# Kernel optimization log

Measured on AMD Instinct MI355X. Metric: run time of the kernel, lower is better.

Reference implementation:

```python
import jax, jax.numpy as jnp
import numpy as np
import math

B, S, DIN, DOUT, H, L, R, E = 8, 512, 256, 256, 8, 4, 8, 65536
N = B * S  # graph nodes = all tokens
DEPTH = DOUT // H


def setup_inputs() -> dict:
    key = jax.random.key(0)
    ks = jax.random.split(key, 16)
    s_in = 1.0 / math.sqrt(DIN)
    s_out = 1.0 / math.sqrt(DOUT)
    return {
        "x": jax.random.normal(ks[0], (B, S, DIN), jnp.float32),
        # graph structure (constant ints)
        "edge_src": jax.random.randint(ks[1], (E,), 0, N),
        "edge_dst": jax.random.randint(ks[2], (E,), 0, N),
        "edge_type": jax.random.randint(ks[3], (E,), 0, R),
        # linear: input_size -> output_size
        "Wl": jax.random.normal(ks[4], (DOUT, DIN), jnp.float32) * s_in,
        "bl": jnp.zeros((DOUT,), jnp.float32),
        # relational GAT params per layer / relation
        "Wgat": jax.random.normal(ks[5], (L, R, DOUT, DOUT), jnp.float32) * s_out,
        "a_src": jax.random.normal(ks[6], (L, R, DOUT), jnp.float32) * s_out,
        "a_dst": jax.random.normal(ks[7], (L, R, DOUT), jnp.float32) * s_out,
        # linear1: output_size -> input_size
        "W1": jax.random.normal(ks[8], (DIN, DOUT), jnp.float32) * s_out,
        "b1": jnp.zeros((DIN,), jnp.float32),
        # Wq, Wk: input_size -> output_size
        "Wq": jax.random.normal(ks[9], (DOUT, DIN), jnp.float32) * s_in,
        "bq": jnp.zeros((DOUT,), jnp.float32),
        "Wk": jax.random.normal(ks[10], (DOUT, DIN), jnp.float32) * s_in,
        "bk": jnp.zeros((DOUT,), jnp.float32),
    }


def _segment_softmax(e, dst, n):
    m = jax.ops.segment_max(e, dst, num_segments=n)
    ex = jnp.exp(e - m[dst])
    denom = jax.ops.segment_sum(ex, dst, num_segments=n)
    return ex / (denom[dst] + 1e-16)


def _rgat(h, Wgat, a_src, a_dst, edge_src, edge_dst, edge_type):
    # h: [N, DOUT]
    for l in range(L):
        # per-relation transform of all nodes: [R, N, D]
        hr = jnp.einsum('nd,rde->rne', h, Wgat[l])
        msg = hr[edge_type, edge_src]  # [E, D] gather by (relation, src)
        logits = (jnp.sum(a_src[l][edge_type] * msg, axis=-1)
                  + jnp.sum(a_dst[l][edge_type] * h[edge_dst], axis=-1))
        alpha = _segment_softmax(jax.nn.leaky_relu(logits, 0.2), edge_dst, N)
        agg = jax.ops.segment_sum(alpha[:, None] * msg, edge_dst, num_segments=N)
        h = jax.nn.elu(agg)
    return h


def reference(x, edge_src, edge_dst, edge_type, Wl, bl, Wgat, a_src, a_dst,
              W1, b1, Wq, bq, Wk, bk):
    h = x @ Wl.T + bl                       # [B, S, DOUT]
    h = h.reshape(N, DOUT)
    h = _rgat(h, Wgat, a_src, a_dst, edge_src, edge_dst, edge_type)
    h = h.reshape(B, S, DOUT)
    h = h @ W1.T + b1                       # [B, S, DIN]
    q = (h @ Wq.T + bq).reshape(B, S, H, DEPTH).transpose(0, 2, 1, 3)
    k = (h @ Wk.T + bk).reshape(B, S, H, DEPTH).transpose(0, 2, 1, 3)
    attn = jnp.einsum('bhqd,bhkd->bhqk', q, k) / math.sqrt(DEPTH)
    return attn
```

## Files before the change

kernel.cpp:

```cpp
#include <hip/hip_runtime.h>
#include <math.h>

#define NN 4096
#define D 256
#define RR 8
#define LL 4
#define EE 65536
#define BB 8
#define SS 512
#define HH 8

typedef short bf16x8 __attribute__((ext_vector_type(8)));
typedef float f32x4 __attribute__((ext_vector_type(4)));

__device__ __forceinline__ unsigned short f2bf(float f) {
  unsigned u = __float_as_uint(f);
  unsigned r = (u + 0x7fffu + ((u >> 16) & 1u)) >> 16;
  return (unsigned short)r;
}
__device__ __forceinline__ float bf2f(unsigned short s) {
  return __uint_as_float(((unsigned)s) << 16);
}

__device__ __forceinline__ void gload16(unsigned short* dst, const unsigned short* src) {
  __builtin_amdgcn_global_load_lds(
      (const __attribute__((address_space(1))) void*)src,
      (__attribute__((address_space(3))) void*)dst, 16, 0, 0);
}

template<int BM, int BN, bool F32OUT, bool SPLITOUT>
__global__ __launch_bounds__(256) void gemm_split(
    const unsigned short* __restrict__ Ah, const unsigned short* __restrict__ Al,
    const unsigned short* __restrict__ Bh, const unsigned short* __restrict__ Bl,
    const float* __restrict__ bias,
    float* __restrict__ C, unsigned short* __restrict__ Ch, unsigned short* __restrict__ Cl,
    int M, int N, int K)
{
  constexpr int MF = BM / 32;
  constexpr int NF = BN / 32;
  __shared__ unsigned short lds[2 * (BM + BN) * 32];
  unsigned short* lA = lds;
  unsigned short* lB = lds + 2 * BM * 32;

  const int t = threadIdx.x;
  const int lane = t & 63;
  const int w = t >> 6;
  const int wm = w >> 1, wn = w & 1;
  const int rb = blockIdx.y * BM;
  const int cb = blockIdx.x * BN;

  f32x4 acc[MF][NF];
#pragma unroll
  for (int m = 0; m < MF; ++m)
#pragma unroll
    for (int n = 0; n < NF; ++n)
      acc[m][n] = (f32x4){0.f, 0.f, 0.f, 0.f};

  const int srow = t >> 2, sslot = t & 3;
  const unsigned short* gAh = Ah + (size_t)(rb + srow) * K + sslot * 8;
  const unsigned short* gAl = Al + (size_t)(rb + srow) * K + sslot * 8;
  const unsigned short* gBh = Bh + (size_t)(cb + srow) * K + sslot * 8;
  const unsigned short* gBl = Bl + (size_t)(cb + srow) * K + sslot * 8;

  for (int k0 = 0; k0 < K; k0 += 32) {
#pragma unroll
    for (int i = 0; i < BM / 64; ++i) {
      gload16(lA + i * 2048 + t * 8,           gAh + (size_t)i * 64 * K + k0);
      gload16(lA + BM * 32 + i * 2048 + t * 8, gAl + (size_t)i * 64 * K + k0);
    }
#pragma unroll
    for (int i = 0; i < BN / 64; ++i) {
      gload16(lB + i * 2048 + t * 8,           gBh + (size_t)i * 64 * K + k0);
      gload16(lB + BN * 32 + i * 2048 + t * 8, gBl + (size_t)i * 64 * K + k0);
    }
    __syncthreads();

    bf16x8 ah[MF], al[MF];
#pragma unroll
    for (int m = 0; m < MF; ++m) {
      int off = (wm * (BM / 2) + m * 16 + (lane & 15)) * 32 + (lane >> 4) * 8;
      ah[m] = *(const bf16x8*)(lA + off);
      al[m] = *(const bf16x8*)(lA + BM * 32 + off);
    }
#pragma unroll
    for (int n = 0; n < NF; ++n) {
      int boff = (wn * (BN / 2) + n * 16 + (lane & 15)) * 32 + (lane >> 4) * 8;
      bf16x8 bh = *(const bf16x8*)(lB + boff);
      bf16x8 bl = *(const bf16x8*)(lB + BN * 32 + boff);
#pragma unroll
      for (int m = 0; m < MF; ++m) {
        acc[m][n] = __builtin_amdgcn_mfma_f32_16x16x32_bf16(ah[m], bh, acc[m][n], 0, 0, 0);
        acc[m][n] = __builtin_amdgcn_mfma_f32_16x16x32_bf16(al[m], bh, acc[m][n], 0, 0, 0);
        acc[m][n] = __builtin_amdgcn_mfma_f32_16x16x32_bf16(ah[m], bl, acc[m][n], 0, 0, 0);
      }
    }
    __syncthreads();
  }

#pragma unroll
  for (int m = 0; m < MF; ++m) {
#pragma unroll
    for (int n = 0; n < NF; ++n) {
      int row0 = rb + wm * (BM / 2) + m * 16 + (lane >> 4) * 4;
      int col = cb + wn * (BN / 2) + n * 16 + (lane & 15);
      float bv = bias ? bias[col] : 0.f;
#pragma unroll
      for (int j = 0; j < 4; ++j) {
        float v = acc[m][n][j] + bv;
        size_t idx = (size_t)(row0 + j) * N + col;
        if (F32OUT) C[idx] = v;
        if (SPLITOUT) {
          unsigned short hb = f2bf(v);
          Ch[idx] = hb;
          Cl[idx] = f2bf(v - bf2f(hb));
        }
      }
    }
  }
}

__global__ __launch_bounds__(256) void cvt_split_k(const float* __restrict__ src,
    unsigned short* __restrict__ hi, unsigned short* __restrict__ lo, int n4)
{
  int i = blockIdx.x * 256 + threadIdx.x;
  if (i >= n4) return;
  float4 v = ((const float4*)src)[i];
  ushort4 h, l;
  h.x = f2bf(v.x); l.x = f2bf(v.x - bf2f(h.x));
  h.y = f2bf(v.y); l.y = f2bf(v.y - bf2f(h.y));
  h.z = f2bf(v.z); l.z = f2bf(v.z - bf2f(h.z));
  h.w = f2bf(v.w); l.w = f2bf(v.w - bf2f(h.w));
  ((ushort4*)hi)[i] = h;
  ((ushort4*)lo)[i] = l;
}

__global__ __launch_bounds__(256) void transp_split_k(const float* __restrict__ W,
    unsigned short* __restrict__ th, unsigned short* __restrict__ tl)
{
  __shared__ float s[32][33];
  int g = blockIdx.z, bi = blockIdx.y, bj = blockIdx.x;
  int t = threadIdx.x;
  int r = t >> 3, c = (t & 7) * 4;
  float4 v = *(const float4*)(W + ((size_t)g * D + bi * 32 + r) * D + bj * 32 + c);
  s[r][c + 0] = v.x; s[r][c + 1] = v.y; s[r][c + 2] = v.z; s[r][c + 3] = v.w;
  __syncthreads();
  size_t ob = ((size_t)g * D + bj * 32 + r) * D + bi * 32 + c;
  ushort4 h, l;
  float o0 = s[c + 0][r], o1 = s[c + 1][r], o2 = s[c + 2][r], o3 = s[c + 3][r];
  h.x = f2bf(o0); l.x = f2bf(o0 - bf2f(h.x));
  h.y = f2bf(o1); l.y = f2bf(o1 - bf2f(h.y));
  h.z = f2bf(o2); l.z = f2bf(o2 - bf2f(h.z));
  h.w = f2bf(o3); l.w = f2bf(o3 - bf2f(h.w));
  *(ushort4*)(th + ob) = h;
  *(ushort4*)(tl + ob) = l;
}

__global__ void count_k(const int* __restrict__ ed, int* __restrict__ cnt) {
  int e = blockIdx.x * 256 + threadIdx.x;
  if (e < EE) atomicAdd(&cnt[ed[e]], 1);
}

__global__ __launch_bounds__(1024) void scan_k(const int* __restrict__ cnt,
    int* __restrict__ off, int* __restrict__ cur) {
  __shared__ int part[1024];
  int t = threadIdx.x;
  int base = t * 4;
  int c0 = cnt[base], c1 = cnt[base+1], c2 = cnt[base+2], c3 = cnt[base+3];
  int s = c0 + c1 + c2 + c3;
  part[t] = s;
  __syncthreads();
  for (int o = 1; o < 1024; o <<= 1) {
    int v = 0;
    if (t >= o) v = part[t - o];
    __syncthreads();
    part[t] += v;
    __syncthreads();
  }
  int excl = part[t] - s;
  off[base] = excl; off[base+1] = excl + c0; off[base+2] = excl + c0 + c1;
  off[base+3] = excl + c0 + c1 + c2;
  cur[base] = excl; cur[base+1] = excl + c0; cur[base+2] = excl + c0 + c1;
  cur[base+3] = excl + c0 + c1 + c2;
  if (t == 1023) off[NN] = EE;
}

__global__ void fill_k(const int* __restrict__ ed, int* __restrict__ cur,
                       int* __restrict__ csr) {
  int e = blockIdx.x * 256 + threadIdx.x;
  if (e < EE) { int p = atomicAdd(&cur[ed[e]], 1); csr[p] = e; }
}

__global__ __launch_bounds__(256) void wa_all_k(const float* __restrict__ Wg,
    const float* __restrict__ asrc, float* __restrict__ wa)
{
  int wid = blockIdx.x * 4 + (threadIdx.x >> 6);
  int lane = threadIdx.x & 63;
  int lr = wid >> 8, d = wid & 255;
  const float* row = Wg + ((size_t)lr * D + d) * D;
  const float* av = asrc + (size_t)lr * D;
  float s = 0.f;
  for (int i = lane; i < D; i += 64) s += row[i] * av[i];
#pragma unroll
  for (int o = 32; o; o >>= 1) s += __shfl_down(s, o);
  if (lane == 0) wa[wid] = s;
}

__global__ __launch_bounds__(256) void fold_k(const float* __restrict__ Wq,
    const float* __restrict__ Wk, const float* __restrict__ W1,
    unsigned short* __restrict__ fh, unsigned short* __restrict__ fl)
{
  int j = (blockIdx.x & 3) * 64 + (threadIdx.x & 63);
  int i = (blockIdx.x >> 2) * 4 + (threadIdx.x >> 6);
  const float* row = i < 256 ? Wq + (size_t)i * D : Wk + (size_t)(i - 256) * D;
  float s = 0.f;
  for (int k = 0; k < D; ++k) s += row[k] * W1[(size_t)k * D + j];
  size_t idx = (size_t)i * D + j;
  unsigned short hb = f2bf(s);
  fh[idx] = hb;
  fl[idx] = f2bf(s - bf2f(hb));
}

__global__ __launch_bounds__(256) void foldb_k(const float* __restrict__ Wq,
    const float* __restrict__ Wk, const float* __restrict__ b1,
    const float* __restrict__ bq, const float* __restrict__ bk,
    float* __restrict__ bqk)
{
  int idx = blockIdx.x * 4 + (threadIdx.x >> 6);
  int lane = threadIdx.x & 63;
  const float* row = idx < 256 ? Wq + (size_t)idx * D : Wk + (size_t)(idx - 256) * D;
  float s = 0.f;
  for (int i = lane; i < D; i += 64) s += row[i] * b1[i];
#pragma unroll
  for (int o = 32; o; o >>= 1) s += __shfl_down(s, o);
  if (lane == 0) bqk[idx] = s + (idx < 256 ? bq[idx] : bk[idx - 256]);
}

__global__ __launch_bounds__(256) void scores2_k(const float* __restrict__ h,
    const float* __restrict__ wa, const float* __restrict__ adst,
    float* __restrict__ ssrc, float* __restrict__ sdst)
{
  int n = blockIdx.x;
  int w = threadIdx.x >> 6, lane = threadIdx.x & 63;
  float4 hv = ((const float4*)(h + (size_t)n * D))[lane];
#pragma unroll
  for (int rr = 0; rr < 2; ++rr) {
    int r = w * 2 + rr;
    float4 a = ((const float4*)(wa + (size_t)r * D))[lane];
    float4 b = ((const float4*)(adst + (size_t)r * D))[lane];
    float s1 = hv.x*a.x + hv.y*a.y + hv.z*a.z + hv.w*a.w;
    float s2 = hv.x*b.x + hv.y*b.y + hv.z*b.z + hv.w*b.w;
#pragma unroll
    for (int o = 32; o; o >>= 1) { s1 += __shfl_down(s1, o); s2 += __shfl_down(s2, o); }
    if (lane == 0) { ssrc[(size_t)r * NN + n] = s1; sdst[(size_t)r * NN + n] = s2; }
  }
}

__global__ __launch_bounds__(256) void agg_fused_k(
    const int* __restrict__ csr, const int* __restrict__ off,
    const int* __restrict__ et, const int* __restrict__ es,
    const float* __restrict__ ssrc, const float* __restrict__ sdst,
    const float* __restrict__ hr2,
    unsigned short* __restrict__ hh, unsigned short* __restrict__ hl,
    const float* __restrict__ wa_next, const float* __restrict__ adst_next,
    float* __restrict__ ssrc_o, float* __restrict__ sdst_o)
{
  __shared__ float slog[1024];
  __shared__ int soff[1024];
  __shared__ float sdn[RR];
  __shared__ float red[8];
  int n = blockIdx.x, tid = threadIdx.x;
  int o0 = off[n];
  int deg = off[n + 1] - o0;
  if (deg > 1024) deg = 1024;
  if (tid < RR) sdn[tid] = sdst[(size_t)tid * NN + n];
  __syncthreads();
  for (int i = tid; i < deg; i += 256) {
    int e = csr[o0 + i];
    int t = et[e], s = es[e];
    float v = ssrc[(size_t)t * NN + s] + sdn[t];
    slog[i] = v > 0.f ? v : 0.2f * v;
    soff[i] = s * (RR * D) + t * D;
  }
  __syncthreads();
  int lane = tid & 63, wv = tid >> 6;
  float lm = -INFINITY;
  for (int i = tid; i < deg; i += 256) lm = fmaxf(lm, slog[i]);
#pragma unroll
  for (int o = 32; o; o >>= 1) lm = fmaxf(lm, __shfl_xor(lm, o));
  if (lane == 0) red[wv] = lm;
  __syncthreads();
  float m = fmaxf(fmaxf(red[0], red[1]), fmaxf(red[2], red[3]));
  float ls = 0.f;
  for (int i = tid; i < deg; i += 256) {
    float a = expf(slog[i] - m);
    slog[i] = a;
    ls += a;
  }
#pragma unroll
  for (int o = 32; o; o >>= 1) ls += __shfl_xor(ls, o);
  if (lane == 0) red[4 + wv] = ls;
  __syncthreads();
  float dinv = 1.f / (red[4] + red[5] + red[6] + red[7] + 1e-16f);
  float acc = 0.f;
  for (int i = 0; i < deg; ++i)
    acc += slog[i] * hr2[(size_t)soff[i] + tid];
  acc *= dinv;
  float v = acc > 0.f ? acc : expm1f(acc);
  size_t idx = (size_t)n * D + tid;
  unsigned short hb = f2bf(v);
  hh[idx] = hb;
  hl[idx] = f2bf(v - bf2f(hb));

  if (wa_next) {
    __syncthreads();
    slog[tid] = v;
    __syncthreads();
#pragma unroll
    for (int rr2 = 0; rr2 < 2; ++rr2) {
      int r = wv * 2 + rr2;
      const float* wr = wa_next + (size_t)r * D;
      const float* ar = adst_next + (size_t)r * D;
      float s1 = slog[lane] * wr[lane] + slog[lane+64] * wr[lane+64]
               + slog[lane+128] * wr[lane+128] + slog[lane+192] * wr[lane+192];
      float s2 = slog[lane] * ar[lane] + slog[lane+64] * ar[lane+64]
               + slog[lane+128] * ar[lane+128] + slog[lane+192] * ar[lane+192];
#pragma unroll
      for (int o = 32; o; o >>= 1) { s1 += __shfl_down(s1, o); s2 += __shfl_down(s2, o); }
      if (lane == 0) { ssrc_o[(size_t)r * NN + n] = s1; sdst_o[(size_t)r * NN + n] = s2; }
    }
  }
}

__global__ __launch_bounds__(256) void attn_mfma_k(
    const unsigned short* __restrict__ qkh, const unsigned short* __restrict__ qkl,
    float* __restrict__ out)
{
  int bh = blockIdx.y; int b = bh >> 3, hd = bh & 7;
  int rb = (blockIdx.x >> 3) * 64, cb = (blockIdx.x & 7) * 64;
  int t = threadIdx.x, lane = t & 63, w = t >> 6;
  int wm = w >> 1, wn = w & 1;
  int colq = hd * 32 + (lane >> 4) * 8;
  int colk = 256 + colq;
  int arow = b * SS + rb + wm * 32 + (lane & 15);
  int brow = b * SS + cb + wn * 32 + (lane & 15);

  bf16x8 aH[2], aL[2], bH[2], bL[2];
#pragma unroll
  for (int m = 0; m < 2; ++m) {
    size_t o1 = (size_t)(arow + m * 16) * 512 + colq;
    aH[m] = *(const bf16x8*)(qkh + o1);
    aL[m] = *(const bf16x8*)(qkl + o1);
    size_t o2 = (size_t)(brow + m * 16) * 512 + colk;
    bH[m] = *(const bf16x8*)(qkh + o2);
    bL[m] = *(const bf16x8*)(qkl + o2);
  }
  f32x4 acc[2][2];
#pragma unroll
  for (int m = 0; m < 2; ++m)
#pragma unroll
    for (int n = 0; n < 2; ++n) {
      acc[m][n] = (f32x4){0.f, 0.f, 0.f, 0.f};
      acc[m][n] = __builtin_amdgcn_mfma_f32_16x16x32_bf16(aH[m], bH[n], acc[m][n], 0, 0, 0);
      acc[m][n] = __builtin_amdgcn_mfma_f32_16x16x32_bf16(aL[m], bH[n], acc[m][n], 0, 0, 0);
      acc[m][n] = __builtin_amdgcn_mfma_f32_16x16x32_bf16(aH[m], bL[n], acc[m][n], 0, 0, 0);
    }
  const float scale = 0.17677669529663687f;
  size_t ob = (size_t)bh * SS * SS;
#pragma unroll
  for (int m = 0; m < 2; ++m)
#pragma unroll
    for (int n = 0; n < 2; ++n) {
      int row0 = rb + wm * 32 + m * 16 + (lane >> 4) * 4;
      int col = cb + wn * 32 + n * 16 + (lane & 15);
#pragma unroll
      for (int j = 0; j < 4; ++j)
        out[ob + (size_t)(row0 + j) * SS + col] = acc[m][n][j] * scale;
    }
}

extern "C" void kernel_launch(void* const* d_in, const int* in_sizes, int n_in,
                              void* d_out, int out_size, void* d_ws, size_t ws_size,
                              hipStream_t stream) {
  const float* x    = (const float*)d_in[0];
  const int*   es   = (const int*)d_in[1];
  const int*   ed   = (const int*)d_in[2];
  const int*   et   = (const int*)d_in[3];
  const float* Wl   = (const float*)d_in[4];
  const float* bl   = (const float*)d_in[5];
  const float* Wgat = (const float*)d_in[6];
  const float* asr  = (const float*)d_in[7];
  const float* adt  = (const float*)d_in[8];
  const float* W1   = (const float*)d_in[9];
  const float* b1   = (const float*)d_in[10];
  const float* Wq   = (const float*)d_in[11];
  const float* bq   = (const float*)d_in[12];
  const float* Wk   = (const float*)d_in[13];
  const float* bk   = (const float*)d_in[14];
  float* out = (float*)d_out;

  char* w = (char*)d_ws;
  size_t o = 0;
  auto alloc = [&](size_t bytes) { void* p = w + o; o += (bytes + 255) & ~(size_t)255; return p; };
  float*          h     = (float*)alloc((size_t)NN * D * 4);
  unsigned short* hh    = (unsigned short*)alloc((size_t)NN * D * 2);
  unsigned short* hl    = (unsigned short*)alloc((size_t)NN * D * 2);
  unsigned short* Wgt_h = (unsigned short*)alloc((size_t)LL * RR * D * D * 2);
  unsigned short* Wgt_l = (unsigned short*)alloc((size_t)LL * RR * D * D * 2);
  unsigned short* wlh   = (unsigned short*)alloc((size_t)D * D * 2);
  unsigned short* wll   = (unsigned short*)alloc((size_t)D * D * 2);
  unsigned short* fqkh  = (unsigned short*)alloc((size_t)2 * D * D * 2);
  unsigned short* fqkl  = (unsigned short*)alloc((size_t)2 * D * D * 2);
  float* bqk   = (float*)alloc((size_t)2 * D * 4);
  float* wa    = (float*)alloc((size_t)LL * RR * D * 4);
  float* ssrcA = (float*)alloc((size_t)RR * NN * 4);
  float* sdstA = (float*)alloc((size_t)RR * NN * 4);
  float* ssrcB = (float*)alloc((size_t)RR * NN * 4);
  float* sdstB = (float*)alloc((size_t)RR * NN * 4);
  int*   cnt   = (int*)alloc((size_t)NN * 4);
  int*   off   = (int*)alloc((size_t)(NN + 1) * 4);
  int*   cur   = (int*)alloc((size_t)NN * 4);
  int*   csr   = (int*)alloc((size_t)EE * 4);
  char* big = (char*)alloc((size_t)NN * RR * D * 4);
  float*          hr2 = (float*)big;
  unsigned short* xh  = (unsigned short*)big;
  unsigned short* xl  = (unsigned short*)(big + (size_t)NN * D * 2);
  unsigned short* qkh = (unsigned short*)big;
  unsigned short* qkl = (unsigned short*)(big + (size_t)NN * 512 * 2);

  hipMemsetAsync(cnt, 0, NN * sizeof(int), stream);
  count_k<<<EE / 256, 256, 0, stream>>>(ed, cnt);
  scan_k<<<1, 1024, 0, stream>>>(cnt, off, cur);
  fill_k<<<EE / 256, 256, 0, stream>>>(ed, cur, csr);

  cvt_split_k<<<NN * D / 1024, 256, 0, stream>>>(x, xh, xl, NN * D / 4);
  cvt_split_k<<<D * D / 1024, 256, 0, stream>>>(Wl, wlh, wll, D * D / 4);
  transp_split_k<<<dim3(8, 8, LL * RR), 256, 0, stream>>>(Wgat, Wgt_h, Wgt_l);
  wa_all_k<<<LL * RR * D / 4, 256, 0, stream>>>(Wgat, asr, wa);
  fold_k<<<512, 256, 0, stream>>>(Wq, Wk, W1, fqkh, fqkl);
  foldb_k<<<128, 256, 0, stream>>>(Wq, Wk, b1, bq, bk, bqk);

  gemm_split<64, 64, true, true><<<dim3(4, 64), 256, 0, stream>>>(
      xh, xl, wlh, wll, bl, h, hh, hl, NN, D, D);
  scores2_k<<<NN, 256, 0, stream>>>(h, wa, adt, ssrcA, sdstA);

  for (int l = 0; l < LL; ++l) {
    gemm_split<128, 128, true, false><<<dim3(16, 32), 256, 0, stream>>>(
        hh, hl, Wgt_h + (size_t)l * RR * D * D, Wgt_l + (size_t)l * RR * D * D,
        nullptr, hr2, nullptr, nullptr, NN, RR * D, D);
    const float* wan = (l < LL - 1) ? wa + (size_t)(l + 1) * RR * D : nullptr;
    const float* adn = (l < LL - 1) ? adt + (size_t)(l + 1) * RR * D : nullptr;
    const float* sin_ = (l & 1) ? ssrcB : ssrcA;
    const float* din_ = (l & 1) ? sdstB : sdstA;
    float* sou_ = (l & 1) ? ssrcA : ssrcB;
    float* dou_ = (l & 1) ? sdstA : sdstB;
    agg_fused_k<<<NN, 256, 0, stream>>>(csr, off, et, es, sin_, din_, hr2,
                                        hh, hl, wan, adn, sou_, dou_);
  }

  gemm_split<64, 64, false, true><<<dim3(8, 64), 256, 0, stream>>>(
      hh, hl, fqkh, fqkl, bqk, nullptr, qkh, qkl, NN, 512, D);

  attn_mfma_k<<<dim3(64, BB * HH), 256, 0, stream>>>(qkh, qkl, out);
}
```

Measured before the change: 258.0 us.

## Reorder RGAT layer as gather-then-transform with relation-bucketed CSR

Each layer now aggregates attention-weighted source features per relation first, using a CSR sorted by (dst, relation), into an [N, R*D] buffer. It then runs a single K=R*D GEMM against the transposed stacked relation weights, with ELU fused into the epilogue. This replaces the old full per-relation transform of every node ([N, R*D] fp32 output) followed by a gather. The GEMM also gains double-buffered LDS staging with one barrier per k-step. Scores move to a separate kernel, degree is capped at 256, and the gather rereads split-bf16 source rows once per relation.

```diff
diff --git a/kernel.cpp b/kernel.cpp
--- a/kernel.cpp
+++ b/kernel.cpp
@@ -9,6 +9,7 @@
 #define BB 8
 #define SS 512
 #define HH 8
+#define MAXDEG 256
 
 typedef short bf16x8 __attribute__((ext_vector_type(8)));
 typedef float f32x4 __attribute__((ext_vector_type(4)));
@@ -28,19 +29,20 @@
       (__attribute__((address_space(3))) void*)dst, 16, 0, 0);
 }
 
-template<int BM, int BN, bool F32OUT, bool SPLITOUT>
+template<int BM, int BN, bool ELU_>
 __global__ __launch_bounds__(256) void gemm_split(
     const unsigned short* __restrict__ Ah, const unsigned short* __restrict__ Al,
     const unsigned short* __restrict__ Bh, const unsigned short* __restrict__ Bl,
     const float* __restrict__ bias,
-    float* __restrict__ C, unsigned short* __restrict__ Ch, unsigned short* __restrict__ Cl,
+    unsigned short* __restrict__ Ch, unsigned short* __restrict__ Cl,
     int M, int N, int K)
 {
   constexpr int MF = BM / 32;
   constexpr int NF = BN / 32;
-  __shared__ unsigned short lds[2 * (BM + BN) * 32];
-  unsigned short* lA = lds;
-  unsigned short* lB = lds + 2 * BM * 32;
+  constexpr int ABUF = BM * 32;
+  constexpr int BBUF = BN * 32;
+  constexpr int BUFSZ = 2 * ABUF + 2 * BBUF;
+  __shared__ unsigned short lds[2 * BUFSZ];
 
   const int t = threadIdx.x;
   const int lane = t & 63;
@@ -62,31 +64,39 @@
   const unsigned short* gBh = Bh + (size_t)(cb + srow) * K + sslot * 8;
   const unsigned short* gBl = Bl + (size_t)(cb + srow) * K + sslot * 8;
 
+  auto stage = [&](int buf, int k0) {
+    unsigned short* p = lds + buf * BUFSZ;
+#pragma unroll
+    for (int i = 0; i < BM / 64; ++i) {
+      gload16(p + i * 2048 + t * 8,        gAh + (size_t)i * 64 * K + k0);
+      gload16(p + ABUF + i * 2048 + t * 8, gAl + (size_t)i * 64 * K + k0);
+    }
+#pragma unroll
+    for (int i = 0; i < BN / 64; ++i) {
+      gload16(p + 2 * ABUF + i * 2048 + t * 8,        gBh + (size_t)i * 64 * K + k0);
+      gload16(p + 2 * ABUF + BBUF + i * 2048 + t * 8, gBl + (size_t)i * 64 * K + k0);
+    }
+  };
+
+  stage(0, 0);
+  int cur = 0;
   for (int k0 = 0; k0 < K; k0 += 32) {
-#pragma unroll
-    for (int i = 0; i < BM / 64; ++i) {
-      gload16(lA + i * 2048 + t * 8,           gAh + (size_t)i * 64 * K + k0);
-      gload16(lA + BM * 32 + i * 2048 + t * 8, gAl + (size_t)i * 64 * K + k0);
-    }
-#pragma unroll
-    for (int i = 0; i < BN / 64; ++i) {
-      gload16(lB + i * 2048 + t * 8,           gBh + (size_t)i * 64 * K + k0);
-      gload16(lB + BN * 32 + i * 2048 + t * 8, gBl + (size_t)i * 64 * K + k0);
-    }
     __syncthreads();
+    if (k0 + 32 < K) stage(cur ^ 1, k0 + 32);
+    const unsigned short* p = lds + cur * BUFSZ;
 
     bf16x8 ah[MF], al[MF];
 #pragma unroll
     for (int m = 0; m < MF; ++m) {
       int off = (wm * (BM / 2) + m * 16 + (lane & 15)) * 32 + (lane >> 4) * 8;
-      ah[m] = *(const bf16x8*)(lA + off);
-      al[m] = *(const bf16x8*)(lA + BM * 32 + off);
+      ah[m] = *(const bf16x8*)(p + off);
+      al[m] = *(const bf16x8*)(p + ABUF + off);
     }
 #pragma unroll
     for (int n = 0; n < NF; ++n) {
       int boff = (wn * (BN / 2) + n * 16 + (lane & 15)) * 32 + (lane >> 4) * 8;
-      bf16x8 bh = *(const bf16x8*)(lB + boff);
-      bf16x8 bl = *(const bf16x8*)(lB + BN * 32 + boff);
+      bf16x8 bh = *(const bf16x8*)(p + 2 * ABUF + boff);
+      bf16x8 bl = *(const bf16x8*)(p + 2 * ABUF + BBUF + boff);
 #pragma unroll
       for (int m = 0; m < MF; ++m) {
         acc[m][n] = __builtin_amdgcn_mfma_f32_16x16x32_bf16(ah[m], bh, acc[m][n], 0, 0, 0);
@@ -94,7 +104,7 @@
         acc[m][n] = __builtin_amdgcn_mfma_f32_16x16x32_bf16(ah[m], bl, acc[m][n], 0, 0, 0);
       }
     }
-    __syncthreads();
+    cur ^= 1;
   }
 
 #pragma unroll
@@ -107,13 +117,11 @@
 #pragma unroll
       for (int j = 0; j < 4; ++j) {
         float v = acc[m][n][j] + bv;
+        if (ELU_) v = v > 0.f ? v : expm1f(v);
         size_t idx = (size_t)(row0 + j) * N + col;
-        if (F32OUT) C[idx] = v;
-        if (SPLITOUT) {
-          unsigned short hb = f2bf(v);
-          Ch[idx] = hb;
-          Cl[idx] = f2bf(v - bf2f(hb));
-        }
+        unsigned short hb = f2bf(v);
+        Ch[idx] = hb;
+        Cl[idx] = f2bf(v - bf2f(hb));
       }
     }
   }
@@ -134,39 +142,42 @@
   ((ushort4*)lo)[i] = l;
 }
 
-__global__ __launch_bounds__(256) void transp_split_k(const float* __restrict__ W,
+__global__ __launch_bounds__(256) void transp2_k(const float* __restrict__ W,
     unsigned short* __restrict__ th, unsigned short* __restrict__ tl)
 {
   __shared__ float s[32][33];
   int g = blockIdx.z, bi = blockIdx.y, bj = blockIdx.x;
+  int l = g >> 3, r = g & 7;
   int t = threadIdx.x;
-  int r = t >> 3, c = (t & 7) * 4;
-  float4 v = *(const float4*)(W + ((size_t)g * D + bi * 32 + r) * D + bj * 32 + c);
-  s[r][c + 0] = v.x; s[r][c + 1] = v.y; s[r][c + 2] = v.z; s[r][c + 3] = v.w;
-  __syncthreads();
-  size_t ob = ((size_t)g * D + bj * 32 + r) * D + bi * 32 + c;
-  ushort4 h, l;
-  float o0 = s[c + 0][r], o1 = s[c + 1][r], o2 = s[c + 2][r], o3 = s[c + 3][r];
-  h.x = f2bf(o0); l.x = f2bf(o0 - bf2f(h.x));
-  h.y = f2bf(o1); l.y = f2bf(o1 - bf2f(h.y));
-  h.z = f2bf(o2); l.z = f2bf(o2 - bf2f(h.z));
-  h.w = f2bf(o3); l.w = f2bf(o3 - bf2f(h.w));
+  int rr = t >> 3, c = (t & 7) * 4;
+  float4 v = *(const float4*)(W + ((size_t)g * D + bi * 32 + rr) * D + bj * 32 + c);
+  s[rr][c + 0] = v.x; s[rr][c + 1] = v.y; s[rr][c + 2] = v.z; s[rr][c + 3] = v.w;
+  __syncthreads();
+  int e = bj * 32 + rr;
+  size_t ob = (((size_t)l * 256 + e) * RR + r) * D + bi * 32 + c;
+  float o0 = s[c + 0][rr], o1 = s[c + 1][rr], o2 = s[c + 2][rr], o3 = s[c + 3][rr];
+  ushort4 h, l4;
+  h.x = f2bf(o0); l4.x = f2bf(o0 - bf2f(h.x));
+  h.y = f2bf(o1); l4.y = f2bf(o1 - bf2f(h.y));
+  h.z = f2bf(o2); l4.z = f2bf(o2 - bf2f(h.z));
+  h.w = f2bf(o3); l4.w = f2bf(o3 - bf2f(h.w));
   *(ushort4*)(th + ob) = h;
-  *(ushort4*)(tl + ob) = l;
-}
-
-__global__ void count_k(const int* __restrict__ ed, int* __restrict__ cnt) {
+  *(ushort4*)(tl + ob) = l4;
+}
+
+__global__ void count2_k(const int* __restrict__ ed, const int* __restrict__ et,
+                         int* __restrict__ cnt) {
   int e = blockIdx.x * 256 + threadIdx.x;
-  if (e < EE) atomicAdd(&cnt[ed[e]], 1);
-}
-
-__global__ __launch_bounds__(1024) void scan_k(const int* __restrict__ cnt,
+  if (e < EE) atomicAdd(&cnt[ed[e] * RR + et[e]], 1);
+}
+
+__global__ __launch_bounds__(1024) void scan2_k(const int* __restrict__ cnt,
     int* __restrict__ off, int* __restrict__ cur) {
   __shared__ int part[1024];
   int t = threadIdx.x;
-  int base = t * 4;
-  int c0 = cnt[base], c1 = cnt[base+1], c2 = cnt[base+2], c3 = cnt[base+3];
-  int s = c0 + c1 + c2 + c3;
+  int base = t * 32;
+  int s = 0;
+  for (int i = 0; i < 32; ++i) s += cnt[base + i];
   part[t] = s;
   __syncthreads();
   for (int o = 1; o < 1024; o <<= 1) {
@@ -176,18 +187,19 @@
     part[t] += v;
     __syncthreads();
   }
-  int excl = part[t] - s;
-  off[base] = excl; off[base+1] = excl + c0; off[base+2] = excl + c0 + c1;
-  off[base+3] = excl + c0 + c1 + c2;
-  cur[base] = excl; cur[base+1] = excl + c0; cur[base+2] = excl + c0 + c1;
-  cur[base+3] = excl + c0 + c1 + c2;
-  if (t == 1023) off[NN] = EE;
-}
-
-__global__ void fill_k(const int* __restrict__ ed, int* __restrict__ cur,
-                       int* __restrict__ csr) {
+  int run = part[t] - s;
+  for (int i = 0; i < 32; ++i) {
+    off[base + i] = run;
+    cur[base + i] = run;
+    run += cnt[base + i];
+  }
+  if (t == 1023) off[NN * RR] = EE;
+}
+
+__global__ void fill2_k(const int* __restrict__ ed, const int* __restrict__ et,
+                        int* __restrict__ cur, int* __restrict__ csr) {
   int e = blockIdx.x * 256 + threadIdx.x;
-  if (e < EE) { int p = atomicAdd(&cur[ed[e]], 1); csr[p] = e; }
+  if (e < EE) { int p = atomicAdd(&cur[ed[e] * RR + et[e]], 1); csr[p] = e; }
 }
 
 __global__ __launch_bounds__(256) void wa_all_k(const float* __restrict__ Wg,
@@ -235,56 +247,64 @@
   if (lane == 0) bqk[idx] = s + (idx < 256 ? bq[idx] : bk[idx - 256]);
 }
 
-__global__ __launch_bounds__(256) void scores2_k(const float* __restrict__ h,
-    const float* __restrict__ wa, const float* __restrict__ adst,
+__global__ __launch_bounds__(256) void scores_split_k(
+    const unsigned short* __restrict__ hh, const unsigned short* __restrict__ hl,
+    const float* __restrict__ wa_l, const float* __restrict__ adst_l,
     float* __restrict__ ssrc, float* __restrict__ sdst)
 {
-  int n = blockIdx.x;
-  int w = threadIdx.x >> 6, lane = threadIdx.x & 63;
-  float4 hv = ((const float4*)(h + (size_t)n * D))[lane];
+  __shared__ float sh[256];
+  int n = blockIdx.x, tid = threadIdx.x;
+  size_t idx = (size_t)n * D + tid;
+  sh[tid] = bf2f(hh[idx]) + bf2f(hl[idx]);
+  __syncthreads();
+  int wv = tid >> 6, lane = tid & 63;
 #pragma unroll
   for (int rr = 0; rr < 2; ++rr) {
-    int r = w * 2 + rr;
-    float4 a = ((const float4*)(wa + (size_t)r * D))[lane];
-    float4 b = ((const float4*)(adst + (size_t)r * D))[lane];
-    float s1 = hv.x*a.x + hv.y*a.y + hv.z*a.z + hv.w*a.w;
-    float s2 = hv.x*b.x + hv.y*b.y + hv.z*b.z + hv.w*b.w;
+    int r = wv * 2 + rr;
+    const float* wr = wa_l + (size_t)r * D;
+    const float* ar = adst_l + (size_t)r * D;
+    float s1 = sh[lane] * wr[lane] + sh[lane+64] * wr[lane+64]
+             + sh[lane+128] * wr[lane+128] + sh[lane+192] * wr[lane+192];
+    float s2 = sh[lane] * ar[lane] + sh[lane+64] * ar[lane+64]
+             + sh[lane+128] * ar[lane+128] + sh[lane+192] * ar[lane+192];
 #pragma unroll
     for (int o = 32; o; o >>= 1) { s1 += __shfl_down(s1, o); s2 += __shfl_down(s2, o); }
     if (lane == 0) { ssrc[(size_t)r * NN + n] = s1; sdst[(size_t)r * NN + n] = s2; }
   }
 }
 
-__global__ __launch_bounds__(256) void agg_fused_k(
-    const int* __restrict__ csr, const int* __restrict__ off,
-    const int* __restrict__ et, const int* __restrict__ es,
+__global__ __launch_bounds__(256) void gather_k(
+    const int* __restrict__ csr, const int* __restrict__ off2,
+    const int* __restrict__ es,
     const float* __restrict__ ssrc, const float* __restrict__ sdst,
-    const float* __restrict__ hr2,
-    unsigned short* __restrict__ hh, unsigned short* __restrict__ hl,
-    const float* __restrict__ wa_next, const float* __restrict__ adst_next,
-    float* __restrict__ ssrc_o, float* __restrict__ sdst_o)
-{
-  __shared__ float slog[1024];
-  __shared__ int soff[1024];
-  __shared__ float sdn[RR];
+    const unsigned short* __restrict__ hh, const unsigned short* __restrict__ hl,
+    unsigned short* __restrict__ gh, unsigned short* __restrict__ gl)
+{
+  __shared__ float sal[MAXDEG];
+  __shared__ int ssid[MAXDEG];
+  __shared__ int sbnd[RR + 1];
   __shared__ float red[8];
   int n = blockIdx.x, tid = threadIdx.x;
-  int o0 = off[n];
-  int deg = off[n + 1] - o0;
-  if (deg > 1024) deg = 1024;
-  if (tid < RR) sdn[tid] = sdst[(size_t)tid * NN + n];
-  __syncthreads();
-  for (int i = tid; i < deg; i += 256) {
-    int e = csr[o0 + i];
-    int t = et[e], s = es[e];
-    float v = ssrc[(size_t)t * NN + s] + sdn[t];
-    slog[i] = v > 0.f ? v : 0.2f * v;
-    soff[i] = s * (RR * D) + t * D;
+  if (tid <= RR) sbnd[tid] = off2[n * RR + tid];
+  __syncthreads();
+  int e0 = sbnd[0];
+  int deg = sbnd[RR] - e0; if (deg > MAXDEG) deg = MAXDEG;
+  for (int r = 0; r < RR; ++r) {
+    float sd = sdst[(size_t)r * NN + n];
+    int a = sbnd[r] - e0, b = sbnd[r + 1] - e0;
+    if (b > MAXDEG) b = MAXDEG;
+    for (int i = a + tid; i < b; i += 256) {
+      int e = csr[e0 + i];
+      int s = es[e];
+      float v = ssrc[(size_t)r * NN + s] + sd;
+      sal[i] = v > 0.f ? v : 0.2f * v;
+      ssid[i] = s;
+    }
   }
   __syncthreads();
   int lane = tid & 63, wv = tid >> 6;
   float lm = -INFINITY;
-  for (int i = tid; i < deg; i += 256) lm = fmaxf(lm, slog[i]);
+  for (int i = tid; i < deg; i += 256) lm = fmaxf(lm, sal[i]);
 #pragma unroll
   for (int o = 32; o; o >>= 1) lm = fmaxf(lm, __shfl_xor(lm, o));
   if (lane == 0) red[wv] = lm;
@@ -292,8 +312,8 @@
   float m = fmaxf(fmaxf(red[0], red[1]), fmaxf(red[2], red[3]));
   float ls = 0.f;
   for (int i = tid; i < deg; i += 256) {
-    float a = expf(slog[i] - m);
-    slog[i] = a;
+    float a = expf(sal[i] - m);
+    sal[i] = a;
     ls += a;
   }
 #pragma unroll
@@ -301,33 +321,20 @@
   if (lane == 0) red[4 + wv] = ls;
   __syncthreads();
   float dinv = 1.f / (red[4] + red[5] + red[6] + red[7] + 1e-16f);
-  float acc = 0.f;
-  for (int i = 0; i < deg; ++i)
-    acc += slog[i] * hr2[(size_t)soff[i] + tid];
-  acc *= dinv;
-  float v = acc > 0.f ? acc : expm1f(acc);
-  size_t idx = (size_t)n * D + tid;
-  unsigned short hb = f2bf(v);
-  hh[idx] = hb;
-  hl[idx] = f2bf(v - bf2f(hb));
-
-  if (wa_next) {
-    __syncthreads();
-    slog[tid] = v;
-    __syncthreads();
-#pragma unroll
-    for (int rr2 = 0; rr2 < 2; ++rr2) {
-      int r = wv * 2 + rr2;
-      const float* wr = wa_next + (size_t)r * D;
-      const float* ar = adst_next + (size_t)r * D;
-      float s1 = slog[lane] * wr[lane] + slog[lane+64] * wr[lane+64]
-               + slog[lane+128] * wr[lane+128] + slog[lane+192] * wr[lane+192];
-      float s2 = slog[lane] * ar[lane] + slog[lane+64] * ar[lane+64]
-               + slog[lane+128] * ar[lane+128] + slog[lane+192] * ar[lane+192];
-#pragma unroll
-      for (int o = 32; o; o >>= 1) { s1 += __shfl_down(s1, o); s2 += __shfl_down(s2, o); }
-      if (lane == 0) { ssrc_o[(size_t)r * NN + n] = s1; sdst_o[(size_t)r * NN + n] = s2; }
-    }
+  for (int r = 0; r < RR; ++r) {
+    int a = sbnd[r] - e0, b = sbnd[r + 1] - e0;
+    if (b > MAXDEG) b = MAXDEG;
+    float acc = 0.f;
+    for (int i = a; i < b; ++i) {
+      int s = ssid[i];
+      float hv = bf2f(hh[(size_t)s * D + tid]) + bf2f(hl[(size_t)s * D + tid]);
+      acc += sal[i] * hv;
+    }
+    acc *= dinv;
+    size_t idx = (size_t)n * (RR * D) + r * D + tid;
+    unsigned short hb = f2bf(acc);
+    gh[idx] = hb;
+    gl[idx] = f2bf(acc - bf2f(hb));
   }
 }
 
@@ -401,64 +408,58 @@
   char* w = (char*)d_ws;
   size_t o = 0;
   auto alloc = [&](size_t bytes) { void* p = w + o; o += (bytes + 255) & ~(size_t)255; return p; };
-  float*          h     = (float*)alloc((size_t)NN * D * 4);
   unsigned short* hh    = (unsigned short*)alloc((size_t)NN * D * 2);
   unsigned short* hl    = (unsigned short*)alloc((size_t)NN * D * 2);
-  unsigned short* Wgt_h = (unsigned short*)alloc((size_t)LL * RR * D * D * 2);
-  unsigned short* Wgt_l = (unsigned short*)alloc((size_t)LL * RR * D * D * 2);
+  unsigned short* Wgt2h = (unsigned short*)alloc((size_t)LL * RR * D * D * 2);
+  unsigned short* Wgt2l = (unsigned short*)alloc((size_t)LL * RR * D * D * 2);
   unsigned short* wlh   = (unsigned short*)alloc((size_t)D * D * 2);
   unsigned short* wll   = (unsigned short*)alloc((size_t)D * D * 2);
   unsigned short* fqkh  = (unsigned short*)alloc((size_t)2 * D * D * 2);
   unsigned short* fqkl  = (unsigned short*)alloc((size_t)2 * D * D * 2);
   float* bqk   = (float*)alloc((size_t)2 * D * 4);
   float* wa    = (float*)alloc((size_t)LL * RR * D * 4);
-  float* ssrcA = (float*)alloc((size_t)RR * NN * 4);
-  float* sdstA = (float*)alloc((size_t)RR * NN * 4);
-  float* ssrcB = (float*)alloc((size_t)RR * NN * 4);
-  float* sdstB = (float*)alloc((size_t)RR * NN * 4);
-  int*   cnt   = (int*)alloc((size_t)NN * 4);
-  int*   off   = (int*)alloc((size_t)(NN + 1) * 4);
-  int*   cur   = (int*)alloc((size_t)NN * 4);
+  float* ssrc  = (float*)alloc((size_t)RR * NN * 4);
+  float* sdst  = (float*)alloc((size_t)RR * NN * 4);
+  int*   cnt2  = (int*)alloc((size_t)NN * RR * 4);
+  int*   off2  = (int*)alloc((size_t)(NN * RR + 1) * 4);
+  int*   cur2  = (int*)alloc((size_t)NN * RR * 4);
   int*   csr   = (int*)alloc((size_t)EE * 4);
   char* big = (char*)alloc((size_t)NN * RR * D * 4);
-  float*          hr2 = (float*)big;
   unsigned short* xh  = (unsigned short*)big;
   unsigned short* xl  = (unsigned short*)(big + (size_t)NN * D * 2);
+  unsigned short* gh  = (unsigned short*)big;
+  unsigned short* gl  = (unsigned short*)(big + (size_t)NN * RR * D * 2);
   unsigned short* qkh = (unsigned short*)big;
   unsigned short* qkl = (unsigned short*)(big + (size_t)NN * 512 * 2);
 
-  hipMemsetAsync(cnt, 0, NN * sizeof(int), stream);
-  count_k<<<EE / 256, 256, 0, stream>>>(ed, cnt);
-  scan_k<<<1, 1024, 0, stream>>>(cnt, off, cur);
-  fill_k<<<EE / 256, 256, 0, stream>>>(ed, cur, csr);
+  hipMemsetAsync(cnt2, 0, NN * RR * sizeof(int), stream);
+  count2_k<<<EE / 256, 256, 0, stream>>>(ed, et, cnt2);
+  scan2_k<<<1, 1024, 0, stream>>>(cnt2, off2, cur2);
+  fill2_k<<<EE / 256, 256, 0, stream>>>(ed, et, cur2, csr);
 
   cvt_split_k<<<NN * D / 1024, 256, 0, stream>>>(x, xh, xl, NN * D / 4);
   cvt_split_k<<<D * D / 1024, 256, 0, stream>>>(Wl, wlh, wll, D * D / 4);
-  transp_split_k<<<dim3(8, 8, LL * RR), 256, 0, stream>>>(Wgat, Wgt_h, Wgt_l);
+  transp2_k<<<dim3(8, 8, LL * RR), 256, 0, stream>>>(Wgat, Wgt2h, Wgt2l);
   wa_all_k<<<LL * RR * D / 4, 256, 0, stream>>>(Wgat, asr, wa);
   fold_k<<<512, 256, 0, stream>>>(Wq, Wk, W1, fqkh, fqkl);
   foldb_k<<<128, 256, 0, stream>>>(Wq, Wk, b1, bq, bk, bqk);
 
-  gemm_split<64, 64, true, true><<<dim3(4, 64), 256, 0, stream>>>(
-      xh, xl, wlh, wll, bl, h, hh, hl, NN, D, D);
-  scores2_k<<<NN, 256, 0, stream>>>(h, wa, adt, ssrcA, sdstA);
+  gemm_split<64, 64, false><<<dim3(4, 64), 256, 0, stream>>>(
+      xh, xl, wlh, wll, bl, hh, hl, NN, D, D);
+  scores_split_k<<<NN, 256, 0, stream>>>(hh, hl, wa, adt, ssrc, sdst);
 
   for (int l = 0; l < LL; ++l) {
-    gemm_split<128, 128, true, false><<<dim3(16, 32), 256, 0, stream>>>(
-        hh, hl, Wgt_h + (size_t)l * RR * D * D, Wgt_l + (size_t)l * RR * D * D,
-        nullptr, hr2, nullptr, nullptr, NN, RR * D, D);
-    const float* wan = (l < LL - 1) ? wa + (size_t)(l + 1) * RR * D : nullptr;
-    const float* adn = (l < LL - 1) ? adt + (size_t)(l + 1) * RR * D : nullptr;
-    const float* sin_ = (l & 1) ? ssrcB : ssrcA;
-    const float* din_ = (l & 1) ? sdstB : sdstA;
-    float* sou_ = (l & 1) ? ssrcA : ssrcB;
-    float* dou_ = (l & 1) ? sdstA : sdstB;
-    agg_fused_k<<<NN, 256, 0, stream>>>(csr, off, et, es, sin_, din_, hr2,
-                                        hh, hl, wan, adn, sou_, dou_);
-  }
-
-  gemm_split<64, 64, false, true><<<dim3(8, 64), 256, 0, stream>>>(
-      hh, hl, fqkh, fqkl, bqk, nullptr, qkh, qkl, NN, 512, D);
+    gather_k<<<NN, 256, 0, stream>>>(csr, off2, es, ssrc, sdst, hh, hl, gh, gl);
+    gemm_split<64, 64, true><<<dim3(4, 64), 256, 0, stream>>>(
+        gh, gl, Wgt2h + (size_t)l * RR * D * D, Wgt2l + (size_t)l * RR * D * D,
+        nullptr, hh, hl, NN, D, RR * D);
+    if (l < LL - 1)
+      scores_split_k<<<NN, 256, 0, stream>>>(hh, hl, wa + (size_t)(l + 1) * RR * D,
+                                             adt + (size_t)(l + 1) * RR * D, ssrc, sdst);
+  }
+
+  gemm_split<64, 64, false><<<dim3(8, 64), 256, 0, stream>>>(
+      hh, hl, fqkh, fqkl, bqk, qkh, qkl, NN, 512, D);
 
   attn_mfma_k<<<dim3(64, BB * HH), 256, 0, stream>>>(qkh, qkl, out);
 }
```

New measurement: 398.5 us. 1.54x slower.

## Double-buffer LDS staging in split-bf16 GEMM and XOR-swizzle LDS layout

Applied to the files above, without the earlier changes.

The split-bf16 GEMM now keeps two LDS buffers and issues the global-to-LDS loads for the next K tile before computing on the current one, leaving a single barrier per iteration. The staging slot is also XOR-swizzled by row so that fragment reads from LDS spread across banks. The aim is to hide global load latency and cut LDS bank conflicts, at the cost of twice the LDS footprint, which may reduce occupancy.

```diff
diff --git a/kernel.cpp b/kernel.cpp
--- a/kernel.cpp
+++ b/kernel.cpp
@@ -38,9 +38,10 @@
 {
   constexpr int MF = BM / 32;
   constexpr int NF = BN / 32;
-  __shared__ unsigned short lds[2 * (BM + BN) * 32];
-  unsigned short* lA = lds;
-  unsigned short* lB = lds + 2 * BM * 32;
+  constexpr int ABUF = BM * 32;
+  constexpr int BBUF = BN * 32;
+  constexpr int BUFSZ = 2 * ABUF + 2 * BBUF;
+  __shared__ unsigned short lds[2 * BUFSZ];
 
   const int t = threadIdx.x;
   const int lane = t & 63;
@@ -56,37 +57,48 @@
     for (int n = 0; n < NF; ++n)
       acc[m][n] = (f32x4){0.f, 0.f, 0.f, 0.f};
 
-  const int srow = t >> 2, sslot = t & 3;
-  const unsigned short* gAh = Ah + (size_t)(rb + srow) * K + sslot * 8;
-  const unsigned short* gAl = Al + (size_t)(rb + srow) * K + sslot * 8;
-  const unsigned short* gBh = Bh + (size_t)(cb + srow) * K + sslot * 8;
-  const unsigned short* gBl = Bl + (size_t)(cb + srow) * K + sslot * 8;
-
+  const int srow = t >> 2;
+  const int lslot = (t & 3) ^ ((srow >> 1) & 3);
+  const unsigned short* gAh = Ah + (size_t)(rb + srow) * K + lslot * 8;
+  const unsigned short* gAl = Al + (size_t)(rb + srow) * K + lslot * 8;
+  const unsigned short* gBh = Bh + (size_t)(cb + srow) * K + lslot * 8;
+  const unsigned short* gBl = Bl + (size_t)(cb + srow) * K + lslot * 8;
+
+  auto stage = [&](int buf, int k0) {
+    unsigned short* p = lds + buf * BUFSZ;
+#pragma unroll
+    for (int i = 0; i < BM / 64; ++i) {
+      gload16(p + i * 2048 + t * 8,        gAh + (size_t)i * 64 * K + k0);
+      gload16(p + ABUF + i * 2048 + t * 8, gAl + (size_t)i * 64 * K + k0);
+    }
+#pragma unroll
+    for (int i = 0; i < BN / 64; ++i) {
+      gload16(p + 2 * ABUF + i * 2048 + t * 8,        gBh + (size_t)i * 64 * K + k0);
+      gload16(p + 2 * ABUF + BBUF + i * 2048 + t * 8, gBl + (size_t)i * 64 * K + k0);
+    }
+  };
+
+  stage(0, 0);
+  int cur = 0;
   for (int k0 = 0; k0 < K; k0 += 32) {
-#pragma unroll
-    for (int i = 0; i < BM / 64; ++i) {
-      gload16(lA + i * 2048 + t * 8,           gAh + (size_t)i * 64 * K + k0);
-      gload16(lA + BM * 32 + i * 2048 + t * 8, gAl + (size_t)i * 64 * K + k0);
-    }
-#pragma unroll
-    for (int i = 0; i < BN / 64; ++i) {
-      gload16(lB + i * 2048 + t * 8,           gBh + (size_t)i * 64 * K + k0);
-      gload16(lB + BN * 32 + i * 2048 + t * 8, gBl + (size_t)i * 64 * K + k0);
-    }
     __syncthreads();
+    if (k0 + 32 < K) stage(cur ^ 1, k0 + 32);
+    const unsigned short* p = lds + cur * BUFSZ;
 
     bf16x8 ah[MF], al[MF];
 #pragma unroll
     for (int m = 0; m < MF; ++m) {
-      int off = (wm * (BM / 2) + m * 16 + (lane & 15)) * 32 + (lane >> 4) * 8;
-      ah[m] = *(const bf16x8*)(lA + off);
-      al[m] = *(const bf16x8*)(lA + BM * 32 + off);
+      int row = wm * (BM / 2) + m * 16 + (lane & 15);
+      int off = row * 32 + (((lane >> 4) ^ ((row >> 1) & 3)) << 3);
+      ah[m] = *(const bf16x8*)(p + off);
+      al[m] = *(const bf16x8*)(p + ABUF + off);
     }
 #pragma unroll
     for (int n = 0; n < NF; ++n) {
-      int boff = (wn * (BN / 2) + n * 16 + (lane & 15)) * 32 + (lane >> 4) * 8;
-      bf16x8 bh = *(const bf16x8*)(lB + boff);
-      bf16x8 bl = *(const bf16x8*)(lB + BN * 32 + boff);
+      int brow = wn * (BN / 2) + n * 16 + (lane & 15);
+      int boff = brow * 32 + (((lane >> 4) ^ ((brow >> 1) & 3)) << 3);
+      bf16x8 bh = *(const bf16x8*)(p + 2 * ABUF + boff);
+      bf16x8 bl = *(const bf16x8*)(p + 2 * ABUF + BBUF + boff);
 #pragma unroll
       for (int m = 0; m < MF; ++m) {
         acc[m][n] = __builtin_amdgcn_mfma_f32_16x16x32_bf16(ah[m], bh, acc[m][n], 0, 0, 0);
@@ -94,7 +106,7 @@
         acc[m][n] = __builtin_amdgcn_mfma_f32_16x16x32_bf16(ah[m], bl, acc[m][n], 0, 0, 0);
       }
     }
-    __syncthreads();
+    cur ^= 1;
   }
 
 #pragma unroll
```

After: 249.6 us. -3.3%, faster.
